# Kernel optimization log

Measured on AMD Instinct MI355X. Metric: run time of the kernel, lower is better.

The kernel has to match this reference:

```python
import jax, jax.numpy as jnp
import numpy as np


def setup_inputs() -> dict:
    key = jax.random.key(0)
    ks = jax.random.split(key, 12)
    B, T, D, H = 256, 512, 128, 256
    s = 0.01
    inp = {
        "x": jax.random.normal(ks[0], (B, T, D), dtype=jnp.float32),
        "h_decay": jax.random.uniform(ks[1], (B, T), dtype=jnp.float32),
        "Wr": jax.random.normal(ks[2], (D, H), dtype=jnp.float32) * s,
        "Wz": jax.random.normal(ks[3], (D, H), dtype=jnp.float32) * s,
        "Wh": jax.random.normal(ks[4], (D, H), dtype=jnp.float32) * s,
        "Ur": jax.random.normal(ks[5], (H, H), dtype=jnp.float32) * s,
        "Uz": jax.random.normal(ks[6], (H, H), dtype=jnp.float32) * s,
        "Uh": jax.random.normal(ks[7], (H, H), dtype=jnp.float32) * s,
        "br": jax.random.normal(ks[8], (H,), dtype=jnp.float32) * s,
        "bz": jax.random.normal(ks[9], (H,), dtype=jnp.float32) * s,
        "bh": jax.random.normal(ks[10], (H,), dtype=jnp.float32) * s,
    }
    return inp


def reference(x, h_decay, Wr, Wz, Wh, Ur, Uz, Uh, br, bz, bh):
    B, T, D = x.shape
    H = Ur.shape[0]
    # Precompute input projections for all timesteps (same math, batched GEMM).
    xz = jnp.einsum("btd,dh->bth", x, Wz) + bz  # [B,T,H]
    xr = jnp.einsum("btd,dh->bth", x, Wr) + br
    xh = jnp.einsum("btd,dh->bth", x, Wh) + bh

    def step(h_tm1, inputs):
        xz_t, xr_t, xh_t, dec_t = inputs
        h_dec = dec_t[:, None] * h_tm1              # decay previous state
        z_t = jax.nn.sigmoid(xz_t + h_dec @ Uz)
        r_t = jax.nn.sigmoid(xr_t + h_dec @ Ur)
        h_prop = jnp.tanh(xh_t + (r_t * h_dec) @ Uh)
        h_t = (1.0 - z_t) * h_dec + z_t * h_prop
        return h_t, h_t

    h0 = jnp.zeros((B, H), dtype=x.dtype)
    scan_inputs = (
        jnp.swapaxes(xz, 0, 1),  # [T,B,H]
        jnp.swapaxes(xr, 0, 1),
        jnp.swapaxes(xh, 0, 1),
        jnp.swapaxes(h_decay, 0, 1),  # [T,B]
    )
    _, hs = jax.lax.scan(step, h0, scan_inputs)
    return jnp.swapaxes(hs, 0, 1)  # [B,T,H]
```

## Files before the change

### kernel.cpp

```cpp
#include <hip/hip_runtime.h>
#include <hip/hip_bf16.h>


static constexpr int Bb = 256;
static constexpr int Tt = 512;
static constexpr int Dd = 128;
static constexpr int Hh = 256;

typedef _Float16 half2_t __attribute__((ext_vector_type(2)));

template<bool BF16OUT>
__global__ __launch_bounds__(256) void proj_kernel(
    const float* __restrict__ x, const float* __restrict__ W,
    const float* __restrict__ bias, void* __restrict__ outv)
{
  __shared__ float xT[Dd][68];
  __shared__ float wS[16][Hh];

  const int tid = threadIdx.x;
  const int ty = tid >> 5;
  const int tx = tid & 31;
  const size_t brow = (size_t)blockIdx.x * 64;
  const float* xp = x + brow * Dd;

  #pragma unroll
  for (int it = 0; it < 8; ++it) {
    int idx = it * 256 + tid;
    int row = idx & 63;
    int kq  = idx >> 6;
    float4 v = *(const float4*)(xp + row * Dd + kq * 4);
    xT[kq * 4 + 0][row] = v.x;
    xT[kq * 4 + 1][row] = v.y;
    xT[kq * 4 + 2][row] = v.z;
    xT[kq * 4 + 3][row] = v.w;
  }

  float bv[8];
  *(float4*)&bv[0] = *(const float4*)(bias + tx * 8);
  *(float4*)&bv[4] = *(const float4*)(bias + tx * 8 + 4);

  float acc[8][8];
  #pragma unroll
  for (int i = 0; i < 8; ++i)
    #pragma unroll
    for (int jj = 0; jj < 8; ++jj) acc[i][jj] = 0.f;

  for (int s = 0; s < 8; ++s) {
    #pragma unroll
    for (int it = 0; it < 4; ++it) {
      int idx = it * 256 + tid;
      int kr = idx >> 6;
      int cq = idx & 63;
      *(float4*)&wS[kr][cq * 4] =
          *(const float4*)(W + (size_t)(s * 16 + kr) * Hh + cq * 4);
    }
    __syncthreads();

    #pragma unroll
    for (int kk = 0; kk < 16; ++kk) {
      const int k = s * 16 + kk;
      float xv[8], wv[8];
      *(float4*)&xv[0] = *(const float4*)&xT[k][ty * 8];
      *(float4*)&xv[4] = *(const float4*)&xT[k][ty * 8 + 4];
      *(float4*)&wv[0] = *(const float4*)&wS[kk][tx * 8];
      *(float4*)&wv[4] = *(const float4*)&wS[kk][tx * 8 + 4];
      #pragma unroll
      for (int i = 0; i < 8; ++i)
        #pragma unroll
        for (int jj = 0; jj < 8; ++jj)
          acc[i][jj] = fmaf(xv[i], wv[jj], acc[i][jj]);
    }
    __syncthreads();
  }

  if (!BF16OUT) {
    float* of = (float*)outv;
    #pragma unroll
    for (int i = 0; i < 8; ++i) {
      size_t ro = (brow + (size_t)ty * 8 + i) * Hh + tx * 8;
      float4 a{acc[i][0] + bv[0], acc[i][1] + bv[1],
               acc[i][2] + bv[2], acc[i][3] + bv[3]};
      float4 c{acc[i][4] + bv[4], acc[i][5] + bv[5],
               acc[i][6] + bv[6], acc[i][7] + bv[7]};
      *(float4*)(of + ro) = a;
      *(float4*)(of + ro + 4) = c;
    }
  } else {
    __hip_bfloat16* ob = (__hip_bfloat16*)outv;
    #pragma unroll
    for (int i = 0; i < 8; ++i) {
      size_t ro = (brow + (size_t)ty * 8 + i) * Hh + tx * 8;
      __hip_bfloat16 tmp[8];
      #pragma unroll
      for (int jj = 0; jj < 8; ++jj)
        tmp[jj] = __float2bfloat16(acc[i][jj] + bv[jj]);
      *(uint4*)(ob + ro) = *(uint4*)tmp;
    }
  }
}

__device__ __forceinline__ float dot2f(unsigned a, unsigned b, float c) {
  half2_t av, bv;
  __builtin_memcpy(&av, &a, 4);
  __builtin_memcpy(&bv, &b, 4);
#if __has_builtin(__builtin_amdgcn_fdot2)
  return __builtin_amdgcn_fdot2(av, bv, c, false);
#else
  return fmaf((float)av[1], (float)bv[1], fmaf((float)av[0], (float)bv[0], c));
#endif
}

__device__ __forceinline__ unsigned packh2(float lo, float hi) {
  half2_t hv;
  hv[0] = (_Float16)lo;
  hv[1] = (_Float16)hi;
  unsigned u;
  __builtin_memcpy(&u, &hv, 4);
  return u;
}

template<bool PROJBF16>
__global__ __launch_bounds__(512, 2) void gru_scan_dot2(
    const void* __restrict__ xz_v, const void* __restrict__ xr_v,
    const float* __restrict__ hdecay,
    const float* __restrict__ Uz, const float* __restrict__ Ur,
    const float* __restrict__ Uh, float* __restrict__ out)
{
  const int tid  = threadIdx.x;
  const int j    = tid & (Hh - 1);
  const int half = tid >> 8;
  const int k0   = half << 7;
  const int b    = blockIdx.x;

  __shared__ unsigned hdp[128];
  __shared__ unsigned rhp[128];
  __shared__ float pz1[Hh], pr1[Hh], ph1[Hh];

  unsigned uz[64], ur[64], uh[64];
  {
    const float* uzp = Uz + (size_t)k0 * Hh + j;
    const float* urp = Ur + (size_t)k0 * Hh + j;
    const float* uhp = Uh + (size_t)k0 * Hh + j;
    #pragma unroll
    for (int m = 0; m < 64; ++m) {
      uz[m] = packh2(uzp[(size_t)(2 * m) * Hh], uzp[(size_t)(2 * m + 1) * Hh]);
      ur[m] = packh2(urp[(size_t)(2 * m) * Hh], urp[(size_t)(2 * m + 1) * Hh]);
      uh[m] = packh2(uhp[(size_t)(2 * m) * Hh], uhp[(size_t)(2 * m + 1) * Hh]);
    }
  }

  if (tid < 128) hdp[tid] = 0u;

  const float* xzf = (const float*)xz_v;
  const float* xrf = (const float*)xr_v;
  const __hip_bfloat16* xzb = (const __hip_bfloat16*)xz_v;
  const __hip_bfloat16* xrb = (const __hip_bfloat16*)xr_v;

  const size_t bbase = (size_t)b * Tt * Hh;
  const int    hbase = b * Tt;

  float hd = 0.f;
  float xz_c = 0.f, xr_c = 0.f, xh_c = 0.f, dec_n = 0.f;

  if (half == 0) {
    if (PROJBF16) {
      xz_c = __bfloat162float(xzb[bbase + j]);
      xr_c = __bfloat162float(xrb[bbase + j]);
    } else {
      xz_c = xzf[bbase + j];
      xr_c = xrf[bbase + j];
    }
    xh_c = out[bbase + j];
    dec_n = hdecay[hbase + 1];
  }
  __syncthreads();

  for (int t = 0; t < Tt; ++t) {
    float xz_n = 0.f, xr_n = 0.f, xh_n = 0.f, dec_n2 = 0.f;
    if (half == 0) {
      const int tp = (t + 1 < Tt) ? t + 1 : Tt - 1;
      const int tq = (t + 2 < Tt) ? t + 2 : Tt - 1;
      const size_t bp = bbase + (size_t)tp * Hh + j;
      if (PROJBF16) {
        xz_n = __bfloat162float(xzb[bp]);
        xr_n = __bfloat162float(xrb[bp]);
      } else {
        xz_n = xzf[bp];
        xr_n = xrf[bp];
      }
      xh_n = out[bp];
      dec_n2 = hdecay[hbase + tq];
    }

    float az0 = 0.f, az1 = 0.f, ar0 = 0.f, ar1 = 0.f;
    #pragma unroll
    for (int m8 = 0; m8 < 64; m8 += 8) {
      uint4 ha = *(const uint4*)&hdp[(half << 6) + m8];
      uint4 hb = *(const uint4*)&hdp[(half << 6) + m8 + 4];
      az0 = dot2f(ha.x, uz[m8 + 0], az0);
      az0 = dot2f(ha.y, uz[m8 + 1], az0);
      az0 = dot2f(ha.z, uz[m8 + 2], az0);
      az0 = dot2f(ha.w, uz[m8 + 3], az0);
      az1 = dot2f(hb.x, uz[m8 + 4], az1);
      az1 = dot2f(hb.y, uz[m8 + 5], az1);
      az1 = dot2f(hb.z, uz[m8 + 6], az1);
      az1 = dot2f(hb.w, uz[m8 + 7], az1);
      ar0 = dot2f(ha.x, ur[m8 + 0], ar0);
      ar0 = dot2f(ha.y, ur[m8 + 1], ar0);
      ar0 = dot2f(ha.z, ur[m8 + 2], ar0);
      ar0 = dot2f(ha.w, ur[m8 + 3], ar0);
      ar1 = dot2f(hb.x, ur[m8 + 4], ar1);
      ar1 = dot2f(hb.y, ur[m8 + 5], ar1);
      ar1 = dot2f(hb.z, ur[m8 + 6], ar1);
      ar1 = dot2f(hb.w, ur[m8 + 7], ar1);
    }
    if (half) { pz1[j] = az0 + az1; pr1[j] = ar0 + ar1; }
    __syncthreads();

    float z = 0.f;
    if (half == 0) {
      float zs = xz_c + az0 + az1 + pz1[j];
      float rs = xr_c + ar0 + ar1 + pr1[j];
      z = 1.f / (1.f + __expf(-zs));
      float r = 1.f / (1.f + __expf(-rs));
      float rh = r * hd;
      float nb = __shfl_xor(rh, 1, 64);
      if ((j & 1) == 0) rhp[j >> 1] = packh2(rh, nb);
    }
    __syncthreads();

    float ah0 = 0.f, ah1 = 0.f;
    #pragma unroll
    for (int m8 = 0; m8 < 64; m8 += 8) {
      uint4 ra = *(const uint4*)&rhp[(half << 6) + m8];
      uint4 rb = *(const uint4*)&rhp[(half << 6) + m8 + 4];
      ah0 = dot2f(ra.x, uh[m8 + 0], ah0);
      ah0 = dot2f(ra.y, uh[m8 + 1], ah0);
      ah0 = dot2f(ra.z, uh[m8 + 2], ah0);
      ah0 = dot2f(ra.w, uh[m8 + 3], ah0);
      ah1 = dot2f(rb.x, uh[m8 + 4], ah1);
      ah1 = dot2f(rb.y, uh[m8 + 5], ah1);
      ah1 = dot2f(rb.z, uh[m8 + 6], ah1);
      ah1 = dot2f(rb.w, uh[m8 + 7], ah1);
    }
    if (half) ph1[j] = ah0 + ah1;
    __syncthreads();

    if (half == 0) {
      float hs = xh_c + ah0 + ah1 + ph1[j];
      float ex = __expf(2.f * hs);
      float hp = 1.f - 2.f / (ex + 1.f);
      float hn = (1.f - z) * hd + z * hp;
      out[bbase + (size_t)t * Hh + j] = hn;
      hd = dec_n * hn;
      float nb = __shfl_xor(hd, 1, 64);
      if ((j & 1) == 0) hdp[j >> 1] = packh2(hd, nb);
      xz_c = xz_n; xr_c = xr_n; xh_c = xh_n; dec_n = dec_n2;
    }
    __syncthreads();
  }
}

extern "C" void kernel_launch(void* const* d_in, const int* in_sizes, int n_in,
                              void* d_out, int out_size, void* d_ws, size_t ws_size,
                              hipStream_t stream) {
  const float* x   = (const float*)d_in[0];
  const float* hdc = (const float*)d_in[1];
  const float* Wr  = (const float*)d_in[2];
  const float* Wz  = (const float*)d_in[3];
  const float* Wh  = (const float*)d_in[4];
  const float* Ur  = (const float*)d_in[5];
  const float* Uz  = (const float*)d_in[6];
  const float* Uh  = (const float*)d_in[7];
  const float* br  = (const float*)d_in[8];
  const float* bz  = (const float*)d_in[9];
  const float* bh  = (const float*)d_in[10];
  float* out = (float*)d_out;

  const size_t bth = (size_t)Bb * Tt * Hh;
  dim3 pgrid(2048), pblk(256);

  proj_kernel<false><<<pgrid, pblk, 0, stream>>>(x, Wh, bh, (void*)out);

  if (ws_size >= bth * 2 * sizeof(float)) {
    float* wsz = (float*)d_ws;
    float* wsr = wsz + bth;
    proj_kernel<false><<<pgrid, pblk, 0, stream>>>(x, Wz, bz, (void*)wsz);
    proj_kernel<false><<<pgrid, pblk, 0, stream>>>(x, Wr, br, (void*)wsr);
    gru_scan_dot2<false><<<dim3(Bb), dim3(512), 0, stream>>>(
        (const void*)wsz, (const void*)wsr, hdc, Uz, Ur, Uh, out);
  } else if (ws_size >= bth * 2 * sizeof(__hip_bfloat16)) {
    __hip_bfloat16* wsz = (__hip_bfloat16*)d_ws;
    __hip_bfloat16* wsr = wsz + bth;
    proj_kernel<true><<<pgrid, pblk, 0, stream>>>(x, Wz, bz, (void*)wsz);
    proj_kernel<true><<<pgrid, pblk, 0, stream>>>(x, Wr, br, (void*)wsr);
    gru_scan_dot2<true><<<dim3(Bb), dim3(512), 0, stream>>>(
        (const void*)wsz, (const void*)wsr, hdc, Uz, Ur, Uh, out);
  }
}
```

Measured before the change: 1.388 ms.

## Fuse three input projections into one fp16 dot2 kernel and rebalance scan gates

Replaces the three separate fp32 projection launches with one kernel that loads x once, packs it and the weights to fp16 pairs, and computes all three gate projections with dot2 instructions. In the recurrent scan, the z and r gate activations are split between the two half-blocks so each half finishes one gate, and the partial sums use four accumulators instead of two. Launch bounds change to one block per CU, and the bf16 workspace fallback path is removed. This cuts x reloads, kernel launches and projection FLOP cost at the price of fp16 precision in the projections and an assumed large workspace.

```diff
diff --git a/kernel.cpp b/kernel.cpp
--- a/kernel.cpp
+++ b/kernel.cpp
@@ -8,96 +8,6 @@
 static constexpr int Hh = 256;
 
 typedef _Float16 half2_t __attribute__((ext_vector_type(2)));
-
-template<bool BF16OUT>
-__global__ __launch_bounds__(256) void proj_kernel(
-    const float* __restrict__ x, const float* __restrict__ W,
-    const float* __restrict__ bias, void* __restrict__ outv)
-{
-  __shared__ float xT[Dd][68];
-  __shared__ float wS[16][Hh];
-
-  const int tid = threadIdx.x;
-  const int ty = tid >> 5;
-  const int tx = tid & 31;
-  const size_t brow = (size_t)blockIdx.x * 64;
-  const float* xp = x + brow * Dd;
-
-  #pragma unroll
-  for (int it = 0; it < 8; ++it) {
-    int idx = it * 256 + tid;
-    int row = idx & 63;
-    int kq  = idx >> 6;
-    float4 v = *(const float4*)(xp + row * Dd + kq * 4);
-    xT[kq * 4 + 0][row] = v.x;
-    xT[kq * 4 + 1][row] = v.y;
-    xT[kq * 4 + 2][row] = v.z;
-    xT[kq * 4 + 3][row] = v.w;
-  }
-
-  float bv[8];
-  *(float4*)&bv[0] = *(const float4*)(bias + tx * 8);
-  *(float4*)&bv[4] = *(const float4*)(bias + tx * 8 + 4);
-
-  float acc[8][8];
-  #pragma unroll
-  for (int i = 0; i < 8; ++i)
-    #pragma unroll
-    for (int jj = 0; jj < 8; ++jj) acc[i][jj] = 0.f;
-
-  for (int s = 0; s < 8; ++s) {
-    #pragma unroll
-    for (int it = 0; it < 4; ++it) {
-      int idx = it * 256 + tid;
-      int kr = idx >> 6;
-      int cq = idx & 63;
-      *(float4*)&wS[kr][cq * 4] =
-          *(const float4*)(W + (size_t)(s * 16 + kr) * Hh + cq * 4);
-    }
-    __syncthreads();
-
-    #pragma unroll
-    for (int kk = 0; kk < 16; ++kk) {
-      const int k = s * 16 + kk;
-      float xv[8], wv[8];
-      *(float4*)&xv[0] = *(const float4*)&xT[k][ty * 8];
-      *(float4*)&xv[4] = *(const float4*)&xT[k][ty * 8 + 4];
-      *(float4*)&wv[0] = *(const float4*)&wS[kk][tx * 8];
-      *(float4*)&wv[4] = *(const float4*)&wS[kk][tx * 8 + 4];
-      #pragma unroll
-      for (int i = 0; i < 8; ++i)
-        #pragma unroll
-        for (int jj = 0; jj < 8; ++jj)
-          acc[i][jj] = fmaf(xv[i], wv[jj], acc[i][jj]);
-    }
-    __syncthreads();
-  }
-
-  if (!BF16OUT) {
-    float* of = (float*)outv;
-    #pragma unroll
-    for (int i = 0; i < 8; ++i) {
-      size_t ro = (brow + (size_t)ty * 8 + i) * Hh + tx * 8;
-      float4 a{acc[i][0] + bv[0], acc[i][1] + bv[1],
-               acc[i][2] + bv[2], acc[i][3] + bv[3]};
-      float4 c{acc[i][4] + bv[4], acc[i][5] + bv[5],
-               acc[i][6] + bv[6], acc[i][7] + bv[7]};
-      *(float4*)(of + ro) = a;
-      *(float4*)(of + ro + 4) = c;
-    }
-  } else {
-    __hip_bfloat16* ob = (__hip_bfloat16*)outv;
-    #pragma unroll
-    for (int i = 0; i < 8; ++i) {
-      size_t ro = (brow + (size_t)ty * 8 + i) * Hh + tx * 8;
-      __hip_bfloat16 tmp[8];
-      #pragma unroll
-      for (int jj = 0; jj < 8; ++jj)
-        tmp[jj] = __float2bfloat16(acc[i][jj] + bv[jj]);
-      *(uint4*)(ob + ro) = *(uint4*)tmp;
-    }
-  }
-}
 
 __device__ __forceinline__ float dot2f(unsigned a, unsigned b, float c) {
   half2_t av, bv;
@@ -119,9 +29,99 @@
   return u;
 }
 
-template<bool PROJBF16>
-__global__ __launch_bounds__(512, 2) void gru_scan_dot2(
-    const void* __restrict__ xz_v, const void* __restrict__ xr_v,
+__global__ __launch_bounds__(256) void proj3_kernel(
+    const float* __restrict__ x,
+    const float* __restrict__ Wz, const float* __restrict__ Wr,
+    const float* __restrict__ Wh,
+    const float* __restrict__ bz, const float* __restrict__ br,
+    const float* __restrict__ bh,
+    float* __restrict__ oz, float* __restrict__ orr, float* __restrict__ oh)
+{
+  __shared__ unsigned xP[64][64];
+  __shared__ unsigned wP[8][256];
+
+  const int tid = threadIdx.x;
+  const int ty = tid >> 5;
+  const int tx = tid & 31;
+  const size_t brow = (size_t)blockIdx.x * 64;
+
+  #pragma unroll
+  for (int it = 0; it < 8; ++it) {
+    int idx = it * 256 + tid;
+    int row = idx & 63;
+    int kq  = idx >> 6;
+    float4 v = *(const float4*)(x + (brow + row) * Dd + kq * 4);
+    xP[kq * 2 + 0][row] = packh2(v.x, v.y);
+    xP[kq * 2 + 1][row] = packh2(v.z, v.w);
+  }
+
+  const float* Ws[3] = {Wz, Wr, Wh};
+  const float* bs[3] = {bz, br, bh};
+  float* os[3] = {oz, orr, oh};
+
+  __syncthreads();
+
+  for (int g = 0; g < 3; ++g) {
+    float bv[8];
+    *(float4*)&bv[0] = *(const float4*)(bs[g] + tx * 8);
+    *(float4*)&bv[4] = *(const float4*)(bs[g] + tx * 8 + 4);
+
+    float acc[8][8];
+    #pragma unroll
+    for (int i = 0; i < 8; ++i)
+      #pragma unroll
+      for (int jj = 0; jj < 8; ++jj) acc[i][jj] = 0.f;
+
+    for (int s = 0; s < 8; ++s) {
+      #pragma unroll
+      for (int it = 0; it < 2; ++it) {
+        int qq  = it * 256 + tid;
+        int kkp = qq >> 6;
+        int c4  = (qq & 63) * 4;
+        const float* wr0 = Ws[g] + (size_t)((s * 8 + kkp) * 2) * Hh + c4;
+        float4 wa = *(const float4*)wr0;
+        float4 wb = *(const float4*)(wr0 + Hh);
+        uint4 pk;
+        pk.x = packh2(wa.x, wb.x);
+        pk.y = packh2(wa.y, wb.y);
+        pk.z = packh2(wa.z, wb.z);
+        pk.w = packh2(wa.w, wb.w);
+        *(uint4*)&wP[kkp][c4] = pk;
+      }
+      __syncthreads();
+
+      #pragma unroll
+      for (int kkp = 0; kkp < 8; ++kkp) {
+        unsigned xv[8], wv[8];
+        *(uint4*)&xv[0] = *(const uint4*)&xP[s * 8 + kkp][ty * 8];
+        *(uint4*)&xv[4] = *(const uint4*)&xP[s * 8 + kkp][ty * 8 + 4];
+        *(uint4*)&wv[0] = *(const uint4*)&wP[kkp][tx * 8];
+        *(uint4*)&wv[4] = *(const uint4*)&wP[kkp][tx * 8 + 4];
+        #pragma unroll
+        for (int i = 0; i < 8; ++i)
+          #pragma unroll
+          for (int jj = 0; jj < 8; ++jj)
+            acc[i][jj] = dot2f(xv[i], wv[jj], acc[i][jj]);
+      }
+      __syncthreads();
+    }
+
+    float* of = os[g];
+    #pragma unroll
+    for (int i = 0; i < 8; ++i) {
+      size_t ro = (brow + (size_t)ty * 8 + i) * Hh + tx * 8;
+      float4 a{acc[i][0] + bv[0], acc[i][1] + bv[1],
+               acc[i][2] + bv[2], acc[i][3] + bv[3]};
+      float4 c{acc[i][4] + bv[4], acc[i][5] + bv[5],
+               acc[i][6] + bv[6], acc[i][7] + bv[7]};
+      *(float4*)(of + ro) = a;
+      *(float4*)(of + ro + 4) = c;
+    }
+  }
+}
+
+__global__ __launch_bounds__(512, 1) void gru_scan_dot2(
+    const float* __restrict__ xz, const float* __restrict__ xr,
     const float* __restrict__ hdecay,
     const float* __restrict__ Uz, const float* __restrict__ Ur,
     const float* __restrict__ Uh, float* __restrict__ out)
@@ -134,7 +134,9 @@
 
   __shared__ unsigned hdp[128];
   __shared__ unsigned rhp[128];
-  __shared__ float pz1[Hh], pr1[Hh], ph1[Hh];
+  __shared__ float pz1[Hh];
+  __shared__ float pr0[Hh];
+  __shared__ float ph1[Hh];
 
   unsigned uz[64], ur[64], uh[64];
   {
@@ -151,11 +153,6 @@
 
   if (tid < 128) hdp[tid] = 0u;
 
-  const float* xzf = (const float*)xz_v;
-  const float* xrf = (const float*)xr_v;
-  const __hip_bfloat16* xzb = (const __hip_bfloat16*)xz_v;
-  const __hip_bfloat16* xrb = (const __hip_bfloat16*)xr_v;
-
   const size_t bbase = (size_t)b * Tt * Hh;
   const int    hbase = b * Tt;
 
@@ -163,91 +160,88 @@
   float xz_c = 0.f, xr_c = 0.f, xh_c = 0.f, dec_n = 0.f;
 
   if (half == 0) {
-    if (PROJBF16) {
-      xz_c = __bfloat162float(xzb[bbase + j]);
-      xr_c = __bfloat162float(xrb[bbase + j]);
-    } else {
-      xz_c = xzf[bbase + j];
-      xr_c = xrf[bbase + j];
-    }
+    xz_c = xz[bbase + j];
     xh_c = out[bbase + j];
     dec_n = hdecay[hbase + 1];
+  } else {
+    xr_c = xr[bbase + j];
   }
   __syncthreads();
 
   for (int t = 0; t < Tt; ++t) {
     float xz_n = 0.f, xr_n = 0.f, xh_n = 0.f, dec_n2 = 0.f;
-    if (half == 0) {
+    {
       const int tp = (t + 1 < Tt) ? t + 1 : Tt - 1;
-      const int tq = (t + 2 < Tt) ? t + 2 : Tt - 1;
       const size_t bp = bbase + (size_t)tp * Hh + j;
-      if (PROJBF16) {
-        xz_n = __bfloat162float(xzb[bp]);
-        xr_n = __bfloat162float(xrb[bp]);
+      if (half == 0) {
+        const int tq = (t + 2 < Tt) ? t + 2 : Tt - 1;
+        xz_n = xz[bp];
+        xh_n = out[bp];
+        dec_n2 = hdecay[hbase + tq];
       } else {
-        xz_n = xzf[bp];
-        xr_n = xrf[bp];
-      }
-      xh_n = out[bp];
-      dec_n2 = hdecay[hbase + tq];
-    }
-
-    float az0 = 0.f, az1 = 0.f, ar0 = 0.f, ar1 = 0.f;
-    #pragma unroll
-    for (int m8 = 0; m8 < 64; m8 += 8) {
-      uint4 ha = *(const uint4*)&hdp[(half << 6) + m8];
-      uint4 hb = *(const uint4*)&hdp[(half << 6) + m8 + 4];
-      az0 = dot2f(ha.x, uz[m8 + 0], az0);
-      az0 = dot2f(ha.y, uz[m8 + 1], az0);
-      az0 = dot2f(ha.z, uz[m8 + 2], az0);
-      az0 = dot2f(ha.w, uz[m8 + 3], az0);
-      az1 = dot2f(hb.x, uz[m8 + 4], az1);
-      az1 = dot2f(hb.y, uz[m8 + 5], az1);
-      az1 = dot2f(hb.z, uz[m8 + 6], az1);
-      az1 = dot2f(hb.w, uz[m8 + 7], az1);
-      ar0 = dot2f(ha.x, ur[m8 + 0], ar0);
-      ar0 = dot2f(ha.y, ur[m8 + 1], ar0);
-      ar0 = dot2f(ha.z, ur[m8 + 2], ar0);
-      ar0 = dot2f(ha.w, ur[m8 + 3], ar0);
-      ar1 = dot2f(hb.x, ur[m8 + 4], ar1);
-      ar1 = dot2f(hb.y, ur[m8 + 5], ar1);
-      ar1 = dot2f(hb.z, ur[m8 + 6], ar1);
-      ar1 = dot2f(hb.w, ur[m8 + 7], ar1);
-    }
-    if (half) { pz1[j] = az0 + az1; pr1[j] = ar0 + ar1; }
+        xr_n = xr[bp];
+      }
+    }
+
+    float az[4] = {0.f, 0.f, 0.f, 0.f};
+    float ar[4] = {0.f, 0.f, 0.f, 0.f};
+    #pragma unroll
+    for (int g4 = 0; g4 < 4; ++g4) {
+      #pragma unroll
+      for (int m4 = 0; m4 < 4; ++m4) {
+        uint4 ha = *(const uint4*)&hdp[(half << 6) + g4 * 16 + m4 * 4];
+        const int mb = g4 * 16 + m4 * 4;
+        az[g4] = dot2f(ha.x, uz[mb + 0], az[g4]);
+        az[g4] = dot2f(ha.y, uz[mb + 1], az[g4]);
+        az[g4] = dot2f(ha.z, uz[mb + 2], az[g4]);
+        az[g4] = dot2f(ha.w, uz[mb + 3], az[g4]);
+        ar[g4] = dot2f(ha.x, ur[mb + 0], ar[g4]);
+        ar[g4] = dot2f(ha.y, ur[mb + 1], ar[g4]);
+        ar[g4] = dot2f(ha.z, ur[mb + 2], ar[g4]);
+        ar[g4] = dot2f(ha.w, ur[mb + 3], ar[g4]);
+      }
+    }
+    const float azs = (az[0] + az[1]) + (az[2] + az[3]);
+    const float ars = (ar[0] + ar[1]) + (ar[2] + ar[3]);
+    if (half) pz1[j] = azs; else pr0[j] = ars;
     __syncthreads();
 
     float z = 0.f;
     if (half == 0) {
-      float zs = xz_c + az0 + az1 + pz1[j];
-      float rs = xr_c + ar0 + ar1 + pr1[j];
+      float zs = xz_c + azs + pz1[j];
       z = 1.f / (1.f + __expf(-zs));
+    } else {
+      float rs = xr_c + ars + pr0[j];
       float r = 1.f / (1.f + __expf(-rs));
-      float rh = r * hd;
+      unsigned hp2 = hdp[j >> 1];
+      half2_t hh;
+      __builtin_memcpy(&hh, &hp2, 4);
+      float hdl = (float)hh[j & 1];
+      float rh = r * hdl;
       float nb = __shfl_xor(rh, 1, 64);
       if ((j & 1) == 0) rhp[j >> 1] = packh2(rh, nb);
     }
     __syncthreads();
 
-    float ah0 = 0.f, ah1 = 0.f;
-    #pragma unroll
-    for (int m8 = 0; m8 < 64; m8 += 8) {
-      uint4 ra = *(const uint4*)&rhp[(half << 6) + m8];
-      uint4 rb = *(const uint4*)&rhp[(half << 6) + m8 + 4];
-      ah0 = dot2f(ra.x, uh[m8 + 0], ah0);
-      ah0 = dot2f(ra.y, uh[m8 + 1], ah0);
-      ah0 = dot2f(ra.z, uh[m8 + 2], ah0);
-      ah0 = dot2f(ra.w, uh[m8 + 3], ah0);
-      ah1 = dot2f(rb.x, uh[m8 + 4], ah1);
-      ah1 = dot2f(rb.y, uh[m8 + 5], ah1);
-      ah1 = dot2f(rb.z, uh[m8 + 6], ah1);
-      ah1 = dot2f(rb.w, uh[m8 + 7], ah1);
-    }
-    if (half) ph1[j] = ah0 + ah1;
+    float ah[4] = {0.f, 0.f, 0.f, 0.f};
+    #pragma unroll
+    for (int g4 = 0; g4 < 4; ++g4) {
+      #pragma unroll
+      for (int m4 = 0; m4 < 4; ++m4) {
+        uint4 ra = *(const uint4*)&rhp[(half << 6) + g4 * 16 + m4 * 4];
+        const int mb = g4 * 16 + m4 * 4;
+        ah[g4] = dot2f(ra.x, uh[mb + 0], ah[g4]);
+        ah[g4] = dot2f(ra.y, uh[mb + 1], ah[g4]);
+        ah[g4] = dot2f(ra.z, uh[mb + 2], ah[g4]);
+        ah[g4] = dot2f(ra.w, uh[mb + 3], ah[g4]);
+      }
+    }
+    const float ahs = (ah[0] + ah[1]) + (ah[2] + ah[3]);
+    if (half) ph1[j] = ahs;
     __syncthreads();
 
     if (half == 0) {
-      float hs = xh_c + ah0 + ah1 + ph1[j];
+      float hs = xh_c + ahs + ph1[j];
       float ex = __expf(2.f * hs);
       float hp = 1.f - 2.f / (ex + 1.f);
       float hn = (1.f - z) * hd + z * hp;
@@ -255,8 +249,8 @@
       hd = dec_n * hn;
       float nb = __shfl_xor(hd, 1, 64);
       if ((j & 1) == 0) hdp[j >> 1] = packh2(hd, nb);
-      xz_c = xz_n; xr_c = xr_n; xh_c = xh_n; dec_n = dec_n2;
-    }
+    }
+    xz_c = xz_n; xr_c = xr_n; xh_c = xh_n; dec_n = dec_n2;
     __syncthreads();
   }
 }
@@ -278,23 +272,12 @@
   float* out = (float*)d_out;
 
   const size_t bth = (size_t)Bb * Tt * Hh;
-  dim3 pgrid(2048), pblk(256);
-
-  proj_kernel<false><<<pgrid, pblk, 0, stream>>>(x, Wh, bh, (void*)out);
-
-  if (ws_size >= bth * 2 * sizeof(float)) {
-    float* wsz = (float*)d_ws;
-    float* wsr = wsz + bth;
-    proj_kernel<false><<<pgrid, pblk, 0, stream>>>(x, Wz, bz, (void*)wsz);
-    proj_kernel<false><<<pgrid, pblk, 0, stream>>>(x, Wr, br, (void*)wsr);
-    gru_scan_dot2<false><<<dim3(Bb), dim3(512), 0, stream>>>(
-        (const void*)wsz, (const void*)wsr, hdc, Uz, Ur, Uh, out);
-  } else if (ws_size >= bth * 2 * sizeof(__hip_bfloat16)) {
-    __hip_bfloat16* wsz = (__hip_bfloat16*)d_ws;
-    __hip_bfloat16* wsr = wsz + bth;
-    proj_kernel<true><<<pgrid, pblk, 0, stream>>>(x, Wz, bz, (void*)wsz);
-    proj_kernel<true><<<pgrid, pblk, 0, stream>>>(x, Wr, br, (void*)wsr);
-    gru_scan_dot2<true><<<dim3(Bb), dim3(512), 0, stream>>>(
-        (const void*)wsz, (const void*)wsr, hdc, Uz, Ur, Uh, out);
-  }
-}
+  float* wsz = (float*)d_ws;
+  float* wsr = wsz + bth;
+
+  proj3_kernel<<<dim3(2048), dim3(256), 0, stream>>>(
+      x, Wz, Wr, Wh, bz, br, bh, wsz, wsr, out);
+
+  gru_scan_dot2<<<dim3(Bb), dim3(512), 0, stream>>>(
+      wsz, wsr, hdc, Uz, Ur, Uh, out);
+}
```

New measurement: 2.298 ms. 1.66x slower.
